# Kernel optimization log

Measured on AMD Instinct MI355X. Metric: run time of the kernel, lower is better.

The kernel has to match this reference:

```python
import jax, jax.numpy as jnp
import numpy as np

B = 512        # batch of parallel sequences
TM1 = 64       # T-1 recurrence steps
BELIEF = 2048  # GRU / deterministic belief size
STATE = 256    # stochastic state size
ACTION = 64
HIDDEN = 2048
EMB = 1024     # embedding_size['fusion']
MIN_STD = 0.1


def setup_inputs() -> dict:
    key = jax.random.key(0)
    ks = jax.random.split(key, 16)
    w = lambda k, shape: jax.random.normal(k, shape, dtype=jnp.float32) * 0.02
    return {
        "prev_state": jax.random.normal(ks[0], (B, STATE), dtype=jnp.float32),
        "actions": jax.random.normal(ks[1], (TM1, B, ACTION), dtype=jnp.float32),
        "prev_belief": jax.random.normal(ks[2], (B, BELIEF), dtype=jnp.float32),
        "obs_emb": jax.random.normal(ks[3], (TM1, B, EMB), dtype=jnp.float32),
        "nonterminals": jnp.ones((TM1, B, 1), dtype=jnp.float32),
        # fc_embed_state_action
        "W_embed": w(ks[4], (STATE + ACTION, BELIEF)),
        "b_embed": jnp.zeros((BELIEF,), jnp.float32),
        # GRUCell (input-to-hidden / hidden-to-hidden, gate order r,z,n as torch)
        "Wi": w(ks[5], (BELIEF, 3 * BELIEF)),
        "bi": jnp.zeros((3 * BELIEF,), jnp.float32),
        "Wh": w(ks[6], (BELIEF, 3 * BELIEF)),
        "bh": jnp.zeros((3 * BELIEF,), jnp.float32),
        # stochastic_state_model (prior): h -> hidden -> 2*state
        "W1": w(ks[7], (BELIEF, HIDDEN)),
        "b1": jnp.zeros((HIDDEN,), jnp.float32),
        "W2": w(ks[8], (HIDDEN, 2 * STATE)),
        "b2": jnp.zeros((2 * STATE,), jnp.float32),
        # obs_encoder (posterior): cat(h, obs_emb) -> hidden -> 2*state
        "W1p": w(ks[9], (BELIEF + EMB, HIDDEN)),
        "b1p": jnp.zeros((HIDDEN,), jnp.float32),
        "W2p": w(ks[10], (HIDDEN, 2 * STATE)),
        "b2p": jnp.zeros((2 * STATE,), jnp.float32),
        # reparameterized-sampling noise (rsample = loc + scale * eps)
        "eps_prior": jax.random.normal(ks[11], (TM1, B, STATE), dtype=jnp.float32),
        "eps_post": jax.random.normal(ks[12], (TM1, B, STATE), dtype=jnp.float32),
    }


def reference(prev_state, actions, prev_belief, obs_emb, nonterminals,
              W_embed, b_embed, Wi, bi, Wh, bh,
              W1, b1, W2, b2, W1p, b1p, W2p, b2p,
              eps_prior, eps_post):
    def step(carry, xs):
        belief, post_state = carry
        a, obs, nt, ep, eq = xs
        s = post_state * nt                                   # [B, S]
        hidden = jax.nn.relu(jnp.concatenate([s, a], axis=1) @ W_embed + b_embed)
        # torch.nn.GRUCell math (gate order r, z, n)
        gi = hidden @ Wi + bi
        gh = belief @ Wh + bh
        i_r, i_z, i_n = jnp.split(gi, 3, axis=1)
        h_r, h_z, h_n = jnp.split(gh, 3, axis=1)
        r = jax.nn.sigmoid(i_r + h_r)
        z = jax.nn.sigmoid(i_z + h_z)
        n = jnp.tanh(i_n + r * h_n)
        new_belief = (1.0 - z) * n + z * belief               # [B, H]
        # prior stochastic state model
        hp = jax.nn.relu(new_belief @ W1 + b1)
        loc_p, raw_p = jnp.split(hp @ W2 + b2, 2, axis=1)
        scale_p = jax.nn.softplus(raw_p) + MIN_STD
        prior_state = loc_p + scale_p * ep                    # rsample
        # posterior from obs embedding
        hq = jax.nn.relu(jnp.concatenate([new_belief, obs], axis=1) @ W1p + b1p)
        loc_q, raw_q = jnp.split(hq @ W2p + b2p, 2, axis=1)
        scale_q = jax.nn.softplus(raw_q) + MIN_STD
        post_new = loc_q + scale_q * eq                       # rsample
        ys = (new_belief, prior_state, loc_p, scale_p, post_new, loc_q, scale_q)
        return (new_belief, post_new), ys

    _, ys = jax.lax.scan(step, (prev_belief, prev_state),
                         (actions, obs_emb, nonterminals, eps_prior, eps_post))
    # (beliefs, prior_states, prior_means, prior_std_devs,
    #  posterior_states, posterior_means, posterior_std_devs), each [T-1, B, ...]
    return ys
```

## Files before the change

### kernel.cpp

```cpp
#include <hip/hip_runtime.h>
#include <hip/hip_bf16.h>
#include <cstdint>

typedef __hip_bfloat16 bf16;
typedef __attribute__((ext_vector_type(8))) short bf16x8v;
typedef __attribute__((ext_vector_type(4))) float f32x4;

#define NB 256
#define NT 512
#define TM1 64

#define OUT_BEL  ((size_t)0)
#define OUT_PST  ((size_t)67108864)
#define OUT_PMU  ((size_t)75497472)
#define OUT_PSD  ((size_t)83886080)
#define OUT_QST  ((size_t)92274688)
#define OUT_QMU  ((size_t)100663296)
#define OUT_QSD  ((size_t)109051904)

__device__ __forceinline__ void gload_lds16(const bf16* g, bf16* l) {
  __builtin_amdgcn_global_load_lds(
      (const __attribute__((address_space(1))) unsigned int*)g,
      (__attribute__((address_space(3))) unsigned int*)l, 16, 0, 0);
}

__device__ __forceinline__ unsigned short bfb(float f) {
  bf16 h = __float2bfloat16(f);
  return *reinterpret_cast<unsigned short*>(&h);
}

__device__ __forceinline__ float sigmoidf_(float x) { return 1.f / (1.f + __expf(-x)); }

__device__ __forceinline__ void gbar(unsigned* bars, unsigned e, int bid) {
  __syncthreads();
  const int g = bid & 7;
  const int tid = threadIdx.x;
  if (tid == 0) {
    __threadfence();
    __hip_atomic_fetch_add(&bars[16 * g], 1u, __ATOMIC_RELAXED, __HIP_MEMORY_SCOPE_AGENT);
  }
  if (bid == 0) {
    if (tid < 8) {
      while (__hip_atomic_load(&bars[16 * tid], __ATOMIC_RELAXED, __HIP_MEMORY_SCOPE_AGENT) < 32u * e)
        __builtin_amdgcn_s_sleep(1);
    }
    __syncthreads();
    if (tid < 8)
      __hip_atomic_store(&bars[128 + 16 * tid], e, __ATOMIC_RELAXED, __HIP_MEMORY_SCOPE_AGENT);
  } else if (tid == 0) {
    while (__hip_atomic_load(&bars[128 + 16 * g], __ATOMIC_RELAXED, __HIP_MEMORY_SCOPE_AGENT) < e)
      __builtin_amdgcn_s_sleep(2);
  }
  if (tid == 0) __threadfence();
  __syncthreads();
}

template<int BM, int BN>
__device__ void gemm_tile(const bf16* __restrict__ A, const bf16* __restrict__ B,
                          const float* __restrict__ bias, void* __restrict__ C,
                          int N, int K, int nm, int mode, int job, int tid,
                          char* pool)
{
  constexpr int LA = BM * 8 / NT;
  constexpr int LB = BN * 8 / NT;
  constexpr int L = LA + LB;
  bf16 (*sA)[BM * 64] = (bf16(*)[BM * 64])pool;
  bf16 (*sB)[BN * 64] = (bf16(*)[BN * 64])(pool + 2 * BM * 64 * 2);

  const int m0 = (job % nm) * BM;
  const int n0 = (job / nm) * BN;
  const int lane = tid & 63;
  const int wid = tid >> 6;
  const int wm = wid >> 1, wn = wid & 1;
  const int lr = lane & 15;
  const int lg = lane >> 4;
  constexpr int WMt = BM / 4, WNt = BN / 2;
  constexpr int MR = WMt / 16, NR = WNt / 16;

  const bf16* Abase = A + (size_t)m0 * K;
  const bf16* Bbase = B + (size_t)n0 * K;

  auto stage = [&](int buf, int k0) {
    #pragma unroll
    for (int i = 0; i < LA; ++i) {
      int c = i * NT + tid;
      int row = c >> 3, kc = c & 7;
      gload_lds16(Abase + (size_t)row * K + k0 + ((kc ^ (row & 7)) << 3), &sA[buf][c * 8]);
    }
    #pragma unroll
    for (int i = 0; i < LB; ++i) {
      int c = i * NT + tid;
      int row = c >> 3, kc = c & 7;
      gload_lds16(Bbase + (size_t)row * K + k0 + ((kc ^ (row & 7)) << 3), &sB[buf][c * 8]);
    }
  };

  f32x4 acc[MR][NR] = {};
  __syncthreads();
  stage(0, 0);
  stage(1, 64);
  const int nk = K >> 6;
  for (int it = 0; it < nk; ++it) {
    const int cur = it & 1;
    if (it + 1 < nk) { asm volatile("s_waitcnt vmcnt(%0)" :: "n"(L) : "memory"); }
    else             { asm volatile("s_waitcnt vmcnt(0)" ::: "memory"); }
    __builtin_amdgcn_sched_barrier(0);
    __builtin_amdgcn_s_barrier();
    __builtin_amdgcn_sched_barrier(0);
    #pragma unroll
    for (int kk = 0; kk < 2; ++kk) {
      const int jg = kk * 4 + lg;
      bf16x8v af[MR], bfv[NR];
      #pragma unroll
      for (int m = 0; m < MR; ++m) {
        int ar = wm * WMt + m * 16 + lr;
        af[m] = *(const bf16x8v*)&sA[cur][ar * 64 + ((jg ^ (ar & 7)) << 3)];
      }
      #pragma unroll
      for (int n = 0; n < NR; ++n) {
        int br = wn * WNt + n * 16 + lr;
        bfv[n] = *(const bf16x8v*)&sB[cur][br * 64 + ((jg ^ (br & 7)) << 3)];
      }
      #pragma unroll
      for (int m = 0; m < MR; ++m)
        #pragma unroll
        for (int n = 0; n < NR; ++n)
          acc[m][n] = __builtin_amdgcn_mfma_f32_16x16x32_bf16(af[m], bfv[n], acc[m][n], 0, 0, 0);
    }
    __builtin_amdgcn_sched_barrier(0);
    __builtin_amdgcn_s_barrier();
    __builtin_amdgcn_sched_barrier(0);
    if (it + 2 < nk) stage(cur, (it + 2) << 6);
  }

  const int r0 = (lane >> 4) * 4;
  #pragma unroll
  for (int m = 0; m < MR; ++m) {
    #pragma unroll
    for (int n = 0; n < NR; ++n) {
      int gc = n0 + wn * WNt + n * 16 + lr;
      float bv = bias[gc];
      #pragma unroll
      for (int r = 0; r < 4; ++r) {
        int gr = m0 + wm * WMt + m * 16 + r0 + r;
        float v = acc[m][n][r] + bv;
        if (mode == 1)
          ((bf16*)C)[(size_t)gr * N + gc] = __float2bfloat16(v > 0.f ? v : 0.f);
        else
          ((float*)C)[(size_t)gr * N + gc] = v;
      }
    }
  }
}

__device__ void fused_gru(const bf16* __restrict__ hidden, const bf16* __restrict__ belsrc,
                          const bf16* __restrict__ WiT, const bf16* __restrict__ WhT,
                          const float* __restrict__ bi, const float* __restrict__ bh,
                          float* __restrict__ belief_f32, float* __restrict__ out_bel,
                          bf16* __restrict__ belslot,
                          int job, int tid, char* pool)
{
  bf16 (*sA)[64 * 64]  = (bf16(*)[64 * 64])pool;
  bf16 (*sB)[192 * 64] = (bf16(*)[192 * 64])(pool + 16384);

  const int m0 = (job & 7) * 64;
  const int j0 = (job >> 3) * 64;
  const int lane = tid & 63;
  const int wid = tid >> 6;
  const int wm = wid >> 2, wn = wid & 3;
  const int lr = lane & 15;
  const int lg = lane >> 4;

  auto stage = [&](int buf, int gt) {
    const bf16* Ab; const bf16* Bb; int k0;
    if (gt < 32) { Ab = hidden; Bb = WiT; k0 = gt << 6; }
    else         { Ab = belsrc; Bb = WhT; k0 = (gt - 32) << 6; }
    {
      int c = tid;
      int row = c >> 3, kc = c & 7;
      gload_lds16(Ab + (size_t)(m0 + row) * 2048 + k0 + ((kc ^ (row & 7)) << 3),
                  &sA[buf][c * 8]);
    }
    #pragma unroll
    for (int i = 0; i < 3; ++i) {
      int c = i * NT + tid;
      int r = c >> 3, kc = c & 7;
      int grow = (r >> 6) * 2048 + j0 + (r & 63);
      gload_lds16(Bb + (size_t)grow * 2048 + k0 + ((kc ^ (r & 7)) << 3),
                  &sB[buf][c * 8]);
    }
  };

  f32x4 ar_[2] = {}, az_[2] = {}, ain[2] = {}, ahn[2] = {};

  auto body = [&](int gt, f32x4 (&ax)[2]) {
    const int cur = gt & 1;
    if (gt < 63) { asm volatile("s_waitcnt vmcnt(4)" ::: "memory"); }
    else         { asm volatile("s_waitcnt vmcnt(0)" ::: "memory"); }
    __builtin_amdgcn_sched_barrier(0);
    __builtin_amdgcn_s_barrier();
    __builtin_amdgcn_sched_barrier(0);
    #pragma unroll
    for (int kk = 0; kk < 2; ++kk) {
      const int jg = kk * 4 + lg;
      bf16x8v af[2], bg[3];
      #pragma unroll
      for (int m = 0; m < 2; ++m) {
        int arow = wm * 32 + m * 16 + lr;
        af[m] = *(const bf16x8v*)&sA[cur][arow * 64 + ((jg ^ (arow & 7)) << 3)];
      }
      #pragma unroll
      for (int g = 0; g < 3; ++g) {
        int br = g * 64 + wn * 16 + lr;
        bg[g] = *(const bf16x8v*)&sB[cur][br * 64 + ((jg ^ (br & 7)) << 3)];
      }
      #pragma unroll
      for (int m = 0; m < 2; ++m) {
        ar_[m] = __builtin_amdgcn_mfma_f32_16x16x32_bf16(af[m], bg[0], ar_[m], 0, 0, 0);
        az_[m] = __builtin_amdgcn_mfma_f32_16x16x32_bf16(af[m], bg[1], az_[m], 0, 0, 0);
        ax[m]  = __builtin_amdgcn_mfma_f32_16x16x32_bf16(af[m], bg[2], ax[m], 0, 0, 0);
      }
    }
    __builtin_amdgcn_sched_barrier(0);
    __builtin_amdgcn_s_barrier();
    __builtin_amdgcn_sched_barrier(0);
    if (gt + 2 < 64) stage(cur, gt + 2);
  };

  __syncthreads();
  stage(0, 0);
  stage(1, 1);
  for (int gt = 0; gt < 32; ++gt) body(gt, ain);
  for (int gt = 32; gt < 64; ++gt) body(gt, ahn);

  const int gc = j0 + wn * 16 + lr;
  const float br_b  = bi[gc] + bh[gc];
  const float bz_b  = bi[2048 + gc] + bh[2048 + gc];
  const float bin_b = bi[4096 + gc];
  const float bhn_b = bh[4096 + gc];
  const int r0 = (lane >> 4) * 4;
  #pragma unroll
  for (int m = 0; m < 2; ++m) {
    #pragma unroll
    for (int r = 0; r < 4; ++r) {
      int grow = m0 + wm * 32 + m * 16 + r0 + r;
      size_t idx = (size_t)grow * 2048 + gc;
      float rr = sigmoidf_(ar_[m][r] + br_b);
      float zz = sigmoidf_(az_[m][r] + bz_b);
      float nn = tanhf(ain[m][r] + bin_b + rr * (ahn[m][r] + bhn_b));
      float bo = belief_f32[idx];
      float nb = (1.f - zz) * nn + zz * bo;
      belief_f32[idx] = nb;
      out_bel[idx] = nb;
      belslot[idx] = __float2bfloat16(nb);
    }
  }
}

__device__ void gemm_w1p(const bf16* __restrict__ Abel, const bf16* __restrict__ Aobs,
                         const bf16* __restrict__ B, const float* __restrict__ bias,
                         bf16* __restrict__ C, int job, int tid, char* pool)
{
  constexpr int K = 3072, NK = 48;
  bf16 (*sA)[64 * 64] = (bf16(*)[64 * 64])pool;
  bf16 (*sB)[64 * 64] = (bf16(*)[64 * 64])(pool + 16384);

  const int m0 = (job & 7) * 64;
  const int n0 = (job >> 3) * 64;
  const int lane = tid & 63;
  const int wid = tid >> 6;
  const int wm = wid >> 1, wn = wid & 1;
  const int lr = lane & 15;
  const int lg = lane >> 4;

  auto stage = [&](int buf, int k0) {
    {
      int c = tid;
      int row = c >> 3, kc = c & 7;
      int sw = (kc ^ (row & 7)) << 3;
      const bf16* src = (k0 < 2048)
          ? Abel + (size_t)(m0 + row) * 2048 + k0 + sw
          : Aobs + (size_t)(m0 + row) * 1024 + (k0 - 2048) + sw;
      gload_lds16(src, &sA[buf][c * 8]);
    }
    {
      int c = tid;
      int row = c >> 3, kc = c & 7;
      gload_lds16(B + (size_t)(n0 + row) * K + k0 + ((kc ^ (row & 7)) << 3), &sB[buf][c * 8]);
    }
  };

  f32x4 acc[2] = {};
  __syncthreads();
  stage(0, 0);
  stage(1, 64);
  for (int it = 0; it < NK; ++it) {
    const int cur = it & 1;
    if (it + 1 < NK) { asm volatile("s_waitcnt vmcnt(2)" ::: "memory"); }
    else             { asm volatile("s_waitcnt vmcnt(0)" ::: "memory"); }
    __builtin_amdgcn_sched_barrier(0);
    __builtin_amdgcn_s_barrier();
    __builtin_amdgcn_sched_barrier(0);
    #pragma unroll
    for (int kk = 0; kk < 2; ++kk) {
      const int jg = kk * 4 + lg;
      int arow = wm * 16 + lr;
      bf16x8v af = *(const bf16x8v*)&sA[cur][arow * 64 + ((jg ^ (arow & 7)) << 3)];
      #pragma unroll
      for (int n = 0; n < 2; ++n) {
        int br = wn * 32 + n * 16 + lr;
        bf16x8v bv = *(const bf16x8v*)&sB[cur][br * 64 + ((jg ^ (br & 7)) << 3)];
        acc[n] = __builtin_amdgcn_mfma_f32_16x16x32_bf16(af, bv, acc[n], 0, 0, 0);
      }
    }
    __builtin_amdgcn_sched_barrier(0);
    __builtin_amdgcn_s_barrier();
    __builtin_amdgcn_sched_barrier(0);
    if (it + 2 < NK) stage(cur, (it + 2) << 6);
  }

  const int r0 = (lane >> 4) * 4;
  #pragma unroll
  for (int n = 0; n < 2; ++n) {
    int gcn = n0 + wn * 32 + n * 16 + lr;
    float bv = bias[gcn];
    #pragma unroll
    for (int r = 0; r < 4; ++r) {
      int gr = m0 + wm * 16 + r0 + r;
      float v = acc[n][r] + bv;
      C[(size_t)gr * 2048 + gcn] = __float2bfloat16(v > 0.f ? v : 0.f);
    }
  }
}

__device__ void w2p_tile(const bf16* __restrict__ hq, const bf16* __restrict__ W2pT,
                         const float* __restrict__ b2p, const float* __restrict__ eps,
                         float* __restrict__ o_mu, float* __restrict__ o_sd,
                         float* __restrict__ o_st,
                         const float* __restrict__ nt_next,
                         const float* __restrict__ act_next,
                         bf16* __restrict__ xcat, int make_xcat,
                         int blk, int tid, char* pool)
{
  constexpr int K = 2048, NK = K / 64;
  const int mb = blk & 7, nl = blk >> 3;
  const int m0 = mb * 64;
  const int j0 = nl * 32;

  bf16 (*sA)[64 * 64] = (bf16(*)[64 * 64])pool;
  bf16 (*sB)[64 * 64] = (bf16(*)[64 * 64])(pool + 16384);
  float* tile = (float*)pool;

  const int lane = tid & 63;
  const int wid = tid >> 6;
  const int wm = wid >> 1, wn = wid & 1;
  const int lr = lane & 15;
  const int lg = lane >> 4;

  const bf16* Abase = hq + (size_t)m0 * K;

  auto stage = [&](int buf, int k0) {
    {
      int c = tid;
      int row = c >> 3, kc = c & 7;
      gload_lds16(Abase + (size_t)row * K + k0 + ((kc ^ (row & 7)) << 3), &sA[buf][c * 8]);
    }
    {
      int c = tid;
      int row = c >> 3, kc = c & 7;
      int grow = (row < 32) ? (j0 + row) : (224 + j0 + row);
      gload_lds16(W2pT + (size_t)grow * K + k0 + ((kc ^ (row & 7)) << 3), &sB[buf][c * 8]);
    }
  };

  f32x4 acc[2] = {};
  __syncthreads();
  stage(0, 0);
  stage(1, 64);
  for (int it = 0; it < NK; ++it) {
    const int cur = it & 1;
    if (it + 1 < NK) { asm volatile("s_waitcnt vmcnt(2)" ::: "memory"); }
    else             { asm volatile("s_waitcnt vmcnt(0)" ::: "memory"); }
    __builtin_amdgcn_sched_barrier(0);
    __builtin_amdgcn_s_barrier();
    __builtin_amdgcn_sched_barrier(0);
    #pragma unroll
    for (int kk = 0; kk < 2; ++kk) {
      const int jg = kk * 4 + lg;
      int ar = wm * 16 + lr;
      bf16x8v af = *(const bf16x8v*)&sA[cur][ar * 64 + ((jg ^ (ar & 7)) << 3)];
      #pragma unroll
      for (int n = 0; n < 2; ++n) {
        int br = wn * 32 + n * 16 + lr;
        bf16x8v bfv = *(const bf16x8v*)&sB[cur][br * 64 + ((jg ^ (br & 7)) << 3)];
        acc[n] = __builtin_amdgcn_mfma_f32_16x16x32_bf16(af, bfv, acc[n], 0, 0, 0);
      }
    }
    __builtin_amdgcn_sched_barrier(0);
    __builtin_amdgcn_s_barrier();
    __builtin_amdgcn_sched_barrier(0);
    if (it + 2 < NK) stage(cur, (it + 2) << 6);
  }

  const int r0 = (lane >> 4) * 4;
  #pragma unroll
  for (int n = 0; n < 2; ++n) {
    int tc = wn * 32 + n * 16 + lr;
    #pragma unroll
    for (int r = 0; r < 4; ++r)
      tile[(wm * 16 + r0 + r) * 64 + tc] = acc[n][r];
  }
  __syncthreads();

  for (int e = tid; e < 64 * 32; e += NT) {
    int rr = e >> 5, cc = e & 31;
    int b = m0 + rr;
    int j = j0 + cc;
    float loc = tile[rr * 64 + cc] + b2p[j];
    float raw = tile[rr * 64 + 32 + cc] + b2p[256 + j];
    float sp = (raw > 20.f) ? raw : log1pf(__expf(raw));
    float scale = sp + 0.1f;
    float st = loc + scale * eps[(size_t)b * 256 + j];
    o_mu[(size_t)b * 256 + j] = loc;
    o_sd[(size_t)b * 256 + j] = scale;
    o_st[(size_t)b * 256 + j] = st;
    if (make_xcat)
      xcat[(size_t)b * 320 + j] = __float2bfloat16(st * nt_next[b]);
  }
  if (make_xcat && nl == 0) {
    for (int e = tid; e < 64 * 64; e += NT) {
      int rr = e >> 6, cc = e & 63;
      int b = m0 + rr;
      xcat[(size_t)b * 320 + 256 + cc] = __float2bfloat16(act_next[(size_t)b * 64 + cc]);
    }
  }
}

__device__ void transpose_phase(const float* __restrict__ src, bf16* __restrict__ dst,
                                int K, int N, int bid, int tid, float* t )
{
  const int ntile = (K / 32) * (N / 32);
  const int tx = tid & 31, ty = tid >> 5;
  for (int it = bid; it < ntile; it += NB) {
    int kt = it % (K / 32), nt = it / (K / 32);
    int k0 = kt * 32, n0 = nt * 32;
    __syncthreads();
    #pragma unroll
    for (int i = 0; i < 32; i += 16)
      t[(ty + i) * 33 + tx] = src[(size_t)(k0 + ty + i) * N + n0 + tx];
    __syncthreads();
    #pragma unroll
    for (int i = 0; i < 32; i += 16)
      dst[(size_t)(n0 + ty + i) * K + k0 + tx] = __float2bfloat16(t[tx * 33 + ty + i]);
  }
}

struct Args {
  const float *prev_state, *actions, *prev_belief, *obs_emb, *nonterm;
  const float *W_embed, *b_embed, *Wi, *bi, *Wh, *bh;
  const float *W1, *b1, *W2, *b2, *W1p, *b1p, *W2p, *b2p;
  const float *eps_p, *eps_q;
  bf16 *WembT, *WiT, *WhT, *W1T, *W2T, *W1pT, *W2pT;
  float* belief_f32; bf16 *bel_init, *xcat, *hidden, *obsB;
  bf16 *hq, *belA, *hp; float* yp;
  float* out;
  unsigned* cnt;
};

__global__ __launch_bounds__(NT, 2) void mega(Args a)
{
  extern __shared__ char pool[];
  const int bid = blockIdx.x;
  const int tid = threadIdx.x;
  const int sj = ((bid & 7) << 5) | (bid >> 3);
  unsigned ep = 0;

  transpose_phase(a.W_embed, a.WembT, 320, 2048, bid, tid, (float*)pool);
  transpose_phase(a.Wi,  a.WiT,  2048, 6144, bid, tid, (float*)pool);
  transpose_phase(a.Wh,  a.WhT,  2048, 6144, bid, tid, (float*)pool);
  transpose_phase(a.W1,  a.W1T,  2048, 2048, bid, tid, (float*)pool);
  transpose_phase(a.W2,  a.W2T,  2048, 512,  bid, tid, (float*)pool);
  transpose_phase(a.W1p, a.W1pT, 3072, 2048, bid, tid, (float*)pool);
  transpose_phase(a.W2p, a.W2pT, 2048, 512,  bid, tid, (float*)pool);
  for (int i = bid * NT + tid; i < 512 * 2048; i += NB * NT) {
    float v = a.prev_belief[i];
    a.belief_f32[i] = v;
    a.bel_init[i] = __float2bfloat16(v);
  }
  for (int i = bid * NT + tid; i < 512 * 320; i += NB * NT) {
    int b = i / 320, c = i - b * 320;
    float v = (c < 256) ? a.prev_state[b * 256 + c] * a.nonterm[b]
                        : a.actions[b * 64 + (c - 256)];
    a.xcat[i] = __float2bfloat16(v);
  }
  for (int i = bid * NT + tid; i < TM1 * 512 * 1024 / 4; i += NB * NT) {
    float4 v = *(const float4*)&a.obs_emb[(size_t)i * 4];
    ushort4 u; u.x = bfb(v.x); u.y = bfb(v.y); u.z = bfb(v.z); u.w = bfb(v.w);
    *(ushort4*)&a.obsB[(size_t)i * 4] = u;
  }
  gbar(a.cnt, ++ep, bid);

  gemm_tile<64, 64>(a.xcat, a.WembT, a.b_embed, a.hidden, 2048, 320, 8, 1, sj, tid, pool);
  gbar(a.cnt, ++ep, bid);

  for (int t = 0; t < TM1; ++t) {
    const bf16* belsrc = (t == 0) ? a.bel_init : a.belA + (size_t)(t - 1) * 512 * 2048;
    fused_gru(a.hidden, belsrc, a.WiT, a.WhT, a.bi, a.bh,
              a.belief_f32,
              a.out + OUT_BEL + (size_t)t * 512 * 2048,
              a.belA + (size_t)t * 512 * 2048,
              sj, tid, pool);
    gbar(a.cnt, ++ep, bid);

    gemm_w1p(a.belA + (size_t)t * 512 * 2048,
             a.obsB + (size_t)t * 512 * 1024,
             a.W1pT, a.b1p, a.hq, sj, tid, pool);
    gbar(a.cnt, ++ep, bid);

    {
      int tn = (t < TM1 - 1) ? t + 1 : t;
      if (bid < 64)
        w2p_tile(a.hq, a.W2pT, a.b2p,
                 a.eps_q + (size_t)t * 512 * 256,
                 a.out + OUT_QMU + (size_t)t * 512 * 256,
                 a.out + OUT_QSD + (size_t)t * 512 * 256,
                 a.out + OUT_QST + (size_t)t * 512 * 256,
                 a.nonterm + (size_t)tn * 512,
                 a.actions + (size_t)tn * 512 * 64,
                 a.xcat, (t < TM1 - 1) ? 1 : 0, bid, tid, pool);
    }
    gbar(a.cnt, ++ep, bid);

    if (t < TM1 - 1) {
      gemm_tile<64, 64>(a.xcat, a.WembT, a.b_embed, a.hidden, 2048, 320, 8, 1, sj, tid, pool);
      gbar(a.cnt, ++ep, bid);
    }
  }

  for (int ch = 0; ch < 8; ++ch) {
    const bf16* Ach = a.belA + (size_t)ch * 4096 * 2048;
    for (int r = 0; r < 2; ++r) {
      int j = r * NB + sj;
      if (j < 512)
        gemm_tile<128, 128>(Ach, a.W1T, a.b1, a.hp, 2048, 2048, 32, 1, j, tid, pool);
    }
    gbar(a.cnt, ++ep, bid);

    if (sj < 128)
      gemm_tile<128, 128>(a.hp, a.W2T, a.b2, a.yp, 512, 2048, 32, 0, sj, tid, pool);
    gbar(a.cnt, ++ep, bid);

    for (int i = bid * NT + tid; i < 4096 * 256; i += NB * NT) {
      int r = i >> 8, j = i & 255;
      float loc = a.yp[(size_t)r * 512 + j];
      float raw = a.yp[(size_t)r * 512 + 256 + j];
      float sp = (raw > 20.f) ? raw : log1pf(__expf(raw));
      float scale = sp + 0.1f;
      size_t o = (size_t)ch * 4096 * 256 + i;
      a.out[OUT_PMU + o] = loc;
      a.out[OUT_PSD + o] = scale;
      a.out[OUT_PST + o] = loc + scale * a.eps_p[o];
    }
    gbar(a.cnt, ++ep, bid);
  }
}

extern "C" void kernel_launch(void* const* d_in, const int* in_sizes, int n_in,
                              void* d_out, int out_size, void* d_ws, size_t ws_size,
                              hipStream_t stream)
{
  (void)in_sizes; (void)n_in; (void)out_size; (void)ws_size;
  Args a;
  a.prev_state = (const float*)d_in[0];
  a.actions    = (const float*)d_in[1];
  a.prev_belief= (const float*)d_in[2];
  a.obs_emb    = (const float*)d_in[3];
  a.nonterm    = (const float*)d_in[4];
  a.W_embed    = (const float*)d_in[5];
  a.b_embed    = (const float*)d_in[6];
  a.Wi         = (const float*)d_in[7];
  a.bi         = (const float*)d_in[8];
  a.Wh         = (const float*)d_in[9];
  a.bh         = (const float*)d_in[10];
  a.W1         = (const float*)d_in[11];
  a.b1         = (const float*)d_in[12];
  a.W2         = (const float*)d_in[13];
  a.b2         = (const float*)d_in[14];
  a.W1p        = (const float*)d_in[15];
  a.b1p        = (const float*)d_in[16];
  a.W2p        = (const float*)d_in[17];
  a.b2p        = (const float*)d_in[18];
  a.eps_p      = (const float*)d_in[19];
  a.eps_q      = (const float*)d_in[20];
  a.out        = (float*)d_out;

  char* ws = (char*)d_ws;
  size_t off = 0;
  auto alloc = [&](size_t bytes) -> char* {
    char* p = ws + off;
    off = (off + bytes + 255) & ~(size_t)255;
    return p;
  };
  a.cnt        = (unsigned*)alloc(4096);
  a.WembT      = (bf16*)alloc((size_t)2048 * 320 * 2);
  a.WiT        = (bf16*)alloc((size_t)6144 * 2048 * 2);
  a.WhT        = (bf16*)alloc((size_t)6144 * 2048 * 2);
  a.W1T        = (bf16*)alloc((size_t)2048 * 2048 * 2);
  a.W2T        = (bf16*)alloc((size_t)512 * 2048 * 2);
  a.W1pT       = (bf16*)alloc((size_t)2048 * 3072 * 2);
  a.W2pT       = (bf16*)alloc((size_t)512 * 2048 * 2);
  a.belief_f32 = (float*)alloc((size_t)512 * 2048 * 4);
  a.bel_init   = (bf16*)alloc((size_t)512 * 2048 * 2);
  a.xcat       = (bf16*)alloc((size_t)512 * 320 * 2);
  a.hidden     = (bf16*)alloc((size_t)512 * 2048 * 2);
  a.obsB       = (bf16*)alloc((size_t)TM1 * 512 * 1024 * 2);
  a.hq         = (bf16*)alloc((size_t)512 * 2048 * 2);
  a.belA       = (bf16*)alloc((size_t)TM1 * 512 * 2048 * 2);
  a.hp         = (bf16*)alloc((size_t)4096 * 2048 * 2);
  a.yp         = (float*)alloc((size_t)4096 * 512 * 4);

  hipMemsetAsync(a.cnt, 0, 4096, stream);
  mega<<<NB, NT, 65536, stream>>>(a);
}
```

Measured before the change: 8.673 ms.

## Enlarge GEMM tiles, add triple-buffered W1p pipeline, and use fewer active blocks

The GRU, W1p and embedding GEMMs move from 64x64-class tiles to 128x128 tiles, and the prior-model GEMMs move to 256x256 tiles. Dynamic LDS is raised to 128 KB to hold the larger tiles, and the W1p GEMM gets a three-deep load pipeline. The goal is to raise MFMA work per loaded byte and cut redundant weight reads across row tiles. The trade-off is that each phase now has only 32–128 jobs instead of 256, so many CUs sit idle while per-block latency grows.

Result: slower. 18.15 ms (+109.3%).

```diff
diff --git a/kernel.cpp b/kernel.cpp
--- a/kernel.cpp
+++ b/kernel.cpp
@@ -31,6 +31,10 @@
 
 __device__ __forceinline__ float sigmoidf_(float x) { return 1.f / (1.f + __expf(-x)); }
 
+__device__ __forceinline__ int jid(int bid, int nj) {
+  return (bid < nj) ? ((bid & 7) * (nj >> 3) + (bid >> 3)) : -1;
+}
+
 __device__ __forceinline__ void gbar(unsigned* bars, unsigned e, int bid) {
   __syncthreads();
   const int g = bid & 7;
@@ -55,7 +59,7 @@
   __syncthreads();
 }
 
-template<int BM, int BN>
+template<int BM, int BN, int DEPTH>
 __device__ void gemm_tile(const bf16* __restrict__ A, const bf16* __restrict__ B,
                           const float* __restrict__ bias, void* __restrict__ C,
                           int N, int K, int nm, int mode, int job, int tid,
@@ -64,8 +68,10 @@
   constexpr int LA = BM * 8 / NT;
   constexpr int LB = BN * 8 / NT;
   constexpr int L = LA + LB;
-  bf16 (*sA)[BM * 64] = (bf16(*)[BM * 64])pool;
-  bf16 (*sB)[BN * 64] = (bf16(*)[BN * 64])(pool + 2 * BM * 64 * 2);
+  constexpr int WMt = BM / 4, WNt = BN / 2;
+  constexpr int MR = WMt / 16, NR = WNt / 16;
+  bf16* sAb = (bf16*)pool;
+  bf16* sBb = (bf16*)(pool + (size_t)DEPTH * BM * 64 * 2);
 
   const int m0 = (job % nm) * BM;
   const int n0 = (job / nm) * BN;
@@ -74,39 +80,48 @@
   const int wm = wid >> 1, wn = wid & 1;
   const int lr = lane & 15;
   const int lg = lane >> 4;
-  constexpr int WMt = BM / 4, WNt = BN / 2;
-  constexpr int MR = WMt / 16, NR = WNt / 16;
 
   const bf16* Abase = A + (size_t)m0 * K;
   const bf16* Bbase = B + (size_t)n0 * K;
 
   auto stage = [&](int buf, int k0) {
+    bf16* dA = sAb + buf * (BM * 64);
+    bf16* dB = sBb + buf * (BN * 64);
     #pragma unroll
     for (int i = 0; i < LA; ++i) {
       int c = i * NT + tid;
       int row = c >> 3, kc = c & 7;
-      gload_lds16(Abase + (size_t)row * K + k0 + ((kc ^ (row & 7)) << 3), &sA[buf][c * 8]);
+      gload_lds16(Abase + (size_t)row * K + k0 + ((kc ^ (row & 7)) << 3), &dA[c * 8]);
     }
     #pragma unroll
     for (int i = 0; i < LB; ++i) {
       int c = i * NT + tid;
       int row = c >> 3, kc = c & 7;
-      gload_lds16(Bbase + (size_t)row * K + k0 + ((kc ^ (row & 7)) << 3), &sB[buf][c * 8]);
+      gload_lds16(Bbase + (size_t)row * K + k0 + ((kc ^ (row & 7)) << 3), &dB[c * 8]);
     }
   };
 
   f32x4 acc[MR][NR] = {};
   __syncthreads();
-  stage(0, 0);
-  stage(1, 64);
   const int nk = K >> 6;
+  #pragma unroll
+  for (int d = 0; d < DEPTH; ++d)
+    if (d < nk) stage(d, d << 6);
+  int cur = 0;
   for (int it = 0; it < nk; ++it) {
-    const int cur = it & 1;
-    if (it + 1 < nk) { asm volatile("s_waitcnt vmcnt(%0)" :: "n"(L) : "memory"); }
-    else             { asm volatile("s_waitcnt vmcnt(0)" ::: "memory"); }
-    __builtin_amdgcn_sched_barrier(0);
-    __builtin_amdgcn_s_barrier();
-    __builtin_amdgcn_sched_barrier(0);
+    if (DEPTH == 3) {
+      if (it + 2 < nk)      { asm volatile("s_waitcnt vmcnt(%0)" :: "n"(2 * L) : "memory"); }
+      else if (it + 1 < nk) { asm volatile("s_waitcnt vmcnt(%0)" :: "n"(L) : "memory"); }
+      else                  { asm volatile("s_waitcnt vmcnt(0)" ::: "memory"); }
+    } else {
+      if (it + 1 < nk)      { asm volatile("s_waitcnt vmcnt(%0)" :: "n"(L) : "memory"); }
+      else                  { asm volatile("s_waitcnt vmcnt(0)" ::: "memory"); }
+    }
+    __builtin_amdgcn_sched_barrier(0);
+    __builtin_amdgcn_s_barrier();
+    __builtin_amdgcn_sched_barrier(0);
+    const bf16* cA = sAb + cur * (BM * 64);
+    const bf16* cB = sBb + cur * (BN * 64);
     #pragma unroll
     for (int kk = 0; kk < 2; ++kk) {
       const int jg = kk * 4 + lg;
@@ -114,12 +129,12 @@
       #pragma unroll
       for (int m = 0; m < MR; ++m) {
         int ar = wm * WMt + m * 16 + lr;
-        af[m] = *(const bf16x8v*)&sA[cur][ar * 64 + ((jg ^ (ar & 7)) << 3)];
+        af[m] = *(const bf16x8v*)&cA[ar * 64 + ((jg ^ (ar & 7)) << 3)];
       }
       #pragma unroll
       for (int n = 0; n < NR; ++n) {
         int br = wn * WNt + n * 16 + lr;
-        bfv[n] = *(const bf16x8v*)&sB[cur][br * 64 + ((jg ^ (br & 7)) << 3)];
+        bfv[n] = *(const bf16x8v*)&cB[br * 64 + ((jg ^ (br & 7)) << 3)];
       }
       #pragma unroll
       for (int m = 0; m < MR; ++m)
@@ -130,7 +145,8 @@
     __builtin_amdgcn_sched_barrier(0);
     __builtin_amdgcn_s_barrier();
     __builtin_amdgcn_sched_barrier(0);
-    if (it + 2 < nk) stage(cur, (it + 2) << 6);
+    if (it + DEPTH < nk) stage(cur, (it + DEPTH) << 6);
+    cur = (cur + 1 == DEPTH) ? 0 : cur + 1;
   }
 
   const int r0 = (lane >> 4) * 4;
@@ -160,14 +176,14 @@
                           bf16* __restrict__ belslot,
                           int job, int tid, char* pool)
 {
-  bf16 (*sA)[64 * 64]  = (bf16(*)[64 * 64])pool;
-  bf16 (*sB)[192 * 64] = (bf16(*)[192 * 64])(pool + 16384);
-
-  const int m0 = (job & 7) * 64;
-  const int j0 = (job >> 3) * 64;
+  bf16 (*sA)[128 * 64] = (bf16(*)[128 * 64])pool;
+  bf16 (*sB)[384 * 64] = (bf16(*)[384 * 64])(pool + 32768);
+
+  const int m0 = (job & 3) * 128;
+  const int j0 = (job >> 2) * 128;
   const int lane = tid & 63;
   const int wid = tid >> 6;
-  const int wm = wid >> 2, wn = wid & 3;
+  const int wm = wid >> 1, wn = wid & 1;
   const int lr = lane & 15;
   const int lg = lane >> 4;
 
@@ -175,27 +191,28 @@
     const bf16* Ab; const bf16* Bb; int k0;
     if (gt < 32) { Ab = hidden; Bb = WiT; k0 = gt << 6; }
     else         { Ab = belsrc; Bb = WhT; k0 = (gt - 32) << 6; }
-    {
-      int c = tid;
+    #pragma unroll
+    for (int i = 0; i < 2; ++i) {
+      int c = i * NT + tid;
       int row = c >> 3, kc = c & 7;
       gload_lds16(Ab + (size_t)(m0 + row) * 2048 + k0 + ((kc ^ (row & 7)) << 3),
                   &sA[buf][c * 8]);
     }
     #pragma unroll
-    for (int i = 0; i < 3; ++i) {
+    for (int i = 0; i < 6; ++i) {
       int c = i * NT + tid;
       int r = c >> 3, kc = c & 7;
-      int grow = (r >> 6) * 2048 + j0 + (r & 63);
+      int grow = (r >> 7) * 2048 + j0 + (r & 127);
       gload_lds16(Bb + (size_t)grow * 2048 + k0 + ((kc ^ (r & 7)) << 3),
                   &sB[buf][c * 8]);
     }
   };
 
-  f32x4 ar_[2] = {}, az_[2] = {}, ain[2] = {}, ahn[2] = {};
-
-  auto body = [&](int gt, f32x4 (&ax)[2]) {
+  f32x4 ar_[2][4] = {}, az_[2][4] = {}, ain[2][4] = {}, ahn[2][4] = {};
+
+  auto body = [&](int gt, f32x4 (&ax)[2][4]) {
     const int cur = gt & 1;
-    if (gt < 63) { asm volatile("s_waitcnt vmcnt(4)" ::: "memory"); }
+    if (gt < 63) { asm volatile("s_waitcnt vmcnt(8)" ::: "memory"); }
     else         { asm volatile("s_waitcnt vmcnt(0)" ::: "memory"); }
     __builtin_amdgcn_sched_barrier(0);
     __builtin_amdgcn_s_barrier();
@@ -203,23 +220,27 @@
     #pragma unroll
     for (int kk = 0; kk < 2; ++kk) {
       const int jg = kk * 4 + lg;
-      bf16x8v af[2], bg[3];
+      bf16x8v af[2], bg[3][4];
       #pragma unroll
       for (int m = 0; m < 2; ++m) {
         int arow = wm * 32 + m * 16 + lr;
         af[m] = *(const bf16x8v*)&sA[cur][arow * 64 + ((jg ^ (arow & 7)) << 3)];
       }
       #pragma unroll
-      for (int g = 0; g < 3; ++g) {
-        int br = g * 64 + wn * 16 + lr;
-        bg[g] = *(const bf16x8v*)&sB[cur][br * 64 + ((jg ^ (br & 7)) << 3)];
-      }
-      #pragma unroll
-      for (int m = 0; m < 2; ++m) {
-        ar_[m] = __builtin_amdgcn_mfma_f32_16x16x32_bf16(af[m], bg[0], ar_[m], 0, 0, 0);
-        az_[m] = __builtin_amdgcn_mfma_f32_16x16x32_bf16(af[m], bg[1], az_[m], 0, 0, 0);
-        ax[m]  = __builtin_amdgcn_mfma_f32_16x16x32_bf16(af[m], bg[2], ax[m], 0, 0, 0);
-      }
+      for (int g = 0; g < 3; ++g)
+        #pragma unroll
+        for (int n = 0; n < 4; ++n) {
+          int br = g * 128 + wn * 64 + n * 16 + lr;
+          bg[g][n] = *(const bf16x8v*)&sB[cur][br * 64 + ((jg ^ (br & 7)) << 3)];
+        }
+      #pragma unroll
+      for (int m = 0; m < 2; ++m)
+        #pragma unroll
+        for (int n = 0; n < 4; ++n) {
+          ar_[m][n] = __builtin_amdgcn_mfma_f32_16x16x32_bf16(af[m], bg[0][n], ar_[m][n], 0, 0, 0);
+          az_[m][n] = __builtin_amdgcn_mfma_f32_16x16x32_bf16(af[m], bg[1][n], az_[m][n], 0, 0, 0);
+          ax[m][n]  = __builtin_amdgcn_mfma_f32_16x16x32_bf16(af[m], bg[2][n], ax[m][n], 0, 0, 0);
+        }
     }
     __builtin_amdgcn_sched_barrier(0);
     __builtin_amdgcn_s_barrier();
@@ -233,26 +254,29 @@
   for (int gt = 0; gt < 32; ++gt) body(gt, ain);
   for (int gt = 32; gt < 64; ++gt) body(gt, ahn);
 
-  const int gc = j0 + wn * 16 + lr;
-  const float br_b  = bi[gc] + bh[gc];
-  const float bz_b  = bi[2048 + gc] + bh[2048 + gc];
-  const float bin_b = bi[4096 + gc];
-  const float bhn_b = bh[4096 + gc];
   const int r0 = (lane >> 4) * 4;
   #pragma unroll
-  for (int m = 0; m < 2; ++m) {
-    #pragma unroll
-    for (int r = 0; r < 4; ++r) {
-      int grow = m0 + wm * 32 + m * 16 + r0 + r;
-      size_t idx = (size_t)grow * 2048 + gc;
-      float rr = sigmoidf_(ar_[m][r] + br_b);
-      float zz = sigmoidf_(az_[m][r] + bz_b);
-      float nn = tanhf(ain[m][r] + bin_b + rr * (ahn[m][r] + bhn_b));
-      float bo = belief_f32[idx];
-      float nb = (1.f - zz) * nn + zz * bo;
-      belief_f32[idx] = nb;
-      out_bel[idx] = nb;
-      belslot[idx] = __float2bfloat16(nb);
+  for (int n = 0; n < 4; ++n) {
+    const int gc = j0 + wn * 64 + n * 16 + lr;
+    const float br_b  = bi[gc] + bh[gc];
+    const float bz_b  = bi[2048 + gc] + bh[2048 + gc];
+    const float bin_b = bi[4096 + gc];
+    const float bhn_b = bh[4096 + gc];
+    #pragma unroll
+    for (int m = 0; m < 2; ++m) {
+      #pragma unroll
+      for (int r = 0; r < 4; ++r) {
+        int grow = m0 + wm * 32 + m * 16 + r0 + r;
+        size_t idx = (size_t)grow * 2048 + gc;
+        float rr = sigmoidf_(ar_[m][n][r] + br_b);
+        float zz = sigmoidf_(az_[m][n][r] + bz_b);
+        float nn = tanhf(ain[m][n][r] + bin_b + rr * (ahn[m][n][r] + bhn_b));
+        float bo = belief_f32[idx];
+        float nb = (1.f - zz) * nn + zz * bo;
+        belief_f32[idx] = nb;
+        out_bel[idx] = nb;
+        belslot[idx] = __float2bfloat16(nb);
+      }
     }
   }
 }
@@ -262,11 +286,11 @@
                          bf16* __restrict__ C, int job, int tid, char* pool)
 {
   constexpr int K = 3072, NK = 48;
-  bf16 (*sA)[64 * 64] = (bf16(*)[64 * 64])pool;
-  bf16 (*sB)[64 * 64] = (bf16(*)[64 * 64])(pool + 16384);
-
-  const int m0 = (job & 7) * 64;
-  const int n0 = (job >> 3) * 64;
+  bf16* sAb = (bf16*)pool;
+  bf16* sBb = (bf16*)(pool + 49152);
+
+  const int m0 = (job & 3) * 128;
+  const int n0 = (job >> 2) * 128;
   const int lane = tid & 63;
   const int wid = tid >> 6;
   const int wm = wid >> 1, wn = wid & 1;
@@ -274,62 +298,79 @@
   const int lg = lane >> 4;
 
   auto stage = [&](int buf, int k0) {
-    {
-      int c = tid;
+    bf16* dA = sAb + buf * (128 * 64);
+    bf16* dB = sBb + buf * (128 * 64);
+    #pragma unroll
+    for (int i = 0; i < 2; ++i) {
+      int c = i * NT + tid;
       int row = c >> 3, kc = c & 7;
       int sw = (kc ^ (row & 7)) << 3;
       const bf16* src = (k0 < 2048)
           ? Abel + (size_t)(m0 + row) * 2048 + k0 + sw
           : Aobs + (size_t)(m0 + row) * 1024 + (k0 - 2048) + sw;
-      gload_lds16(src, &sA[buf][c * 8]);
-    }
-    {
-      int c = tid;
+      gload_lds16(src, &dA[c * 8]);
+    }
+    #pragma unroll
+    for (int i = 0; i < 2; ++i) {
+      int c = i * NT + tid;
       int row = c >> 3, kc = c & 7;
-      gload_lds16(B + (size_t)(n0 + row) * K + k0 + ((kc ^ (row & 7)) << 3), &sB[buf][c * 8]);
+      gload_lds16(B + (size_t)(n0 + row) * K + k0 + ((kc ^ (row & 7)) << 3), &dB[c * 8]);
     }
   };
 
-  f32x4 acc[2] = {};
+  f32x4 acc[2][4] = {};
   __syncthreads();
-  stage(0, 0);
-  stage(1, 64);
+  stage(0, 0); stage(1, 64); stage(2, 128);
+  int cur = 0;
   for (int it = 0; it < NK; ++it) {
-    const int cur = it & 1;
-    if (it + 1 < NK) { asm volatile("s_waitcnt vmcnt(2)" ::: "memory"); }
-    else             { asm volatile("s_waitcnt vmcnt(0)" ::: "memory"); }
-    __builtin_amdgcn_sched_barrier(0);
-    __builtin_amdgcn_s_barrier();
-    __builtin_amdgcn_sched_barrier(0);
+    if (it + 2 < NK)      { asm volatile("s_waitcnt vmcnt(8)" ::: "memory"); }
+    else if (it + 1 < NK) { asm volatile("s_waitcnt vmcnt(4)" ::: "memory"); }
+    else                  { asm volatile("s_waitcnt vmcnt(0)" ::: "memory"); }
+    __builtin_amdgcn_sched_barrier(0);
+    __builtin_amdgcn_s_barrier();
+    __builtin_amdgcn_sched_barrier(0);
+    const bf16* cA = sAb + cur * (128 * 64);
+    const bf16* cB = sBb + cur * (128 * 64);
     #pragma unroll
     for (int kk = 0; kk < 2; ++kk) {
       const int jg = kk * 4 + lg;
-      int arow = wm * 16 + lr;
-      bf16x8v af = *(const bf16x8v*)&sA[cur][arow * 64 + ((jg ^ (arow & 7)) << 3)];
-      #pragma unroll
-      for (int n = 0; n < 2; ++n) {
-        int br = wn * 32 + n * 16 + lr;
-        bf16x8v bv = *(const bf16x8v*)&sB[cur][br * 64 + ((jg ^ (br & 7)) << 3)];
-        acc[n] = __builtin_amdgcn_mfma_f32_16x16x32_bf16(af, bv, acc[n], 0, 0, 0);
-      }
-    }
-    __builtin_amdgcn_sched_barrier(0);
-    __builtin_amdgcn_s_barrier();
-    __builtin_amdgcn_sched_barrier(0);
-    if (it + 2 < NK) stage(cur, (it + 2) << 6);
+      bf16x8v af[2], bfv[4];
+      #pragma unroll
+      for (int m = 0; m < 2; ++m) {
+        int ar = wm * 32 + m * 16 + lr;
+        af[m] = *(const bf16x8v*)&cA[ar * 64 + ((jg ^ (ar & 7)) << 3)];
+      }
+      #pragma unroll
+      for (int n = 0; n < 4; ++n) {
+        int br = wn * 64 + n * 16 + lr;
+        bfv[n] = *(const bf16x8v*)&cB[br * 64 + ((jg ^ (br & 7)) << 3)];
+      }
+      #pragma unroll
+      for (int m = 0; m < 2; ++m)
+        #pragma unroll
+        for (int n = 0; n < 4; ++n)
+          acc[m][n] = __builtin_amdgcn_mfma_f32_16x16x32_bf16(af[m], bfv[n], acc[m][n], 0, 0, 0);
+    }
+    __builtin_amdgcn_sched_barrier(0);
+    __builtin_amdgcn_s_barrier();
+    __builtin_amdgcn_sched_barrier(0);
+    if (it + 3 < NK) stage(cur, (it + 3) << 6);
+    cur = (cur + 1 == 3) ? 0 : cur + 1;
   }
 
   const int r0 = (lane >> 4) * 4;
   #pragma unroll
-  for (int n = 0; n < 2; ++n) {
-    int gcn = n0 + wn * 32 + n * 16 + lr;
+  for (int n = 0; n < 4; ++n) {
+    int gcn = n0 + wn * 64 + n * 16 + lr;
     float bv = bias[gcn];
     #pragma unroll
-    for (int r = 0; r < 4; ++r) {
-      int gr = m0 + wm * 16 + r0 + r;
-      float v = acc[n][r] + bv;
-      C[(size_t)gr * 2048 + gcn] = __float2bfloat16(v > 0.f ? v : 0.f);
-    }
+    for (int m = 0; m < 2; ++m)
+      #pragma unroll
+      for (int r = 0; r < 4; ++r) {
+        int gr = m0 + wm * 32 + m * 16 + r0 + r;
+        float v = acc[m][n][r] + bv;
+        C[(size_t)gr * 2048 + gcn] = __float2bfloat16(v > 0.f ? v : 0.f);
+      }
   }
 }
 
@@ -472,7 +513,6 @@
   extern __shared__ char pool[];
   const int bid = blockIdx.x;
   const int tid = threadIdx.x;
-  const int sj = ((bid & 7) << 5) | (bid >> 3);
   unsigned ep = 0;
 
   transpose_phase(a.W_embed, a.WembT, 320, 2048, bid, tid, (float*)pool);
@@ -500,21 +540,33 @@
   }
   gbar(a.cnt, ++ep, bid);
 
-  gemm_tile<64, 64>(a.xcat, a.WembT, a.b_embed, a.hidden, 2048, 320, 8, 1, sj, tid, pool);
+  {
+    int j = jid(bid, 64);
+    if (j >= 0)
+      gemm_tile<128, 128, 2>(a.xcat, a.WembT, a.b_embed, a.hidden, 2048, 320, 4, 1, j, tid, pool);
+  }
   gbar(a.cnt, ++ep, bid);
 
   for (int t = 0; t < TM1; ++t) {
     const bf16* belsrc = (t == 0) ? a.bel_init : a.belA + (size_t)(t - 1) * 512 * 2048;
-    fused_gru(a.hidden, belsrc, a.WiT, a.WhT, a.bi, a.bh,
-              a.belief_f32,
-              a.out + OUT_BEL + (size_t)t * 512 * 2048,
-              a.belA + (size_t)t * 512 * 2048,
-              sj, tid, pool);
+    {
+      int j = jid(bid, 64);
+      if (j >= 0)
+        fused_gru(a.hidden, belsrc, a.WiT, a.WhT, a.bi, a.bh,
+                  a.belief_f32,
+                  a.out + OUT_BEL + (size_t)t * 512 * 2048,
+                  a.belA + (size_t)t * 512 * 2048,
+                  j, tid, pool);
+    }
     gbar(a.cnt, ++ep, bid);
 
-    gemm_w1p(a.belA + (size_t)t * 512 * 2048,
-             a.obsB + (size_t)t * 512 * 1024,
-             a.W1pT, a.b1p, a.hq, sj, tid, pool);
+    {
+      int j = jid(bid, 64);
+      if (j >= 0)
+        gemm_w1p(a.belA + (size_t)t * 512 * 2048,
+                 a.obsB + (size_t)t * 512 * 1024,
+                 a.W1pT, a.b1p, a.hq, j, tid, pool);
+    }
     gbar(a.cnt, ++ep, bid);
 
     {
@@ -532,22 +584,27 @@
     gbar(a.cnt, ++ep, bid);
 
     if (t < TM1 - 1) {
-      gemm_tile<64, 64>(a.xcat, a.WembT, a.b_embed, a.hidden, 2048, 320, 8, 1, sj, tid, pool);
+      int j = jid(bid, 64);
+      if (j >= 0)
+        gemm_tile<128, 128, 2>(a.xcat, a.WembT, a.b_embed, a.hidden, 2048, 320, 4, 1, j, tid, pool);
       gbar(a.cnt, ++ep, bid);
     }
   }
 
   for (int ch = 0; ch < 8; ++ch) {
     const bf16* Ach = a.belA + (size_t)ch * 4096 * 2048;
-    for (int r = 0; r < 2; ++r) {
-      int j = r * NB + sj;
-      if (j < 512)
-        gemm_tile<128, 128>(Ach, a.W1T, a.b1, a.hp, 2048, 2048, 32, 1, j, tid, pool);
+    {
+      int j = jid(bid, 128);
+      if (j >= 0)
+        gemm_tile<256, 256, 2>(Ach, a.W1T, a.b1, a.hp, 2048, 2048, 16, 1, j, tid, pool);
     }
     gbar(a.cnt, ++ep, bid);
 
-    if (sj < 128)
-      gemm_tile<128, 128>(a.hp, a.W2T, a.b2, a.yp, 512, 2048, 32, 0, sj, tid, pool);
+    {
+      int j = jid(bid, 32);
+      if (j >= 0)
+        gemm_tile<256, 256, 2>(a.hp, a.W2T, a.b2, a.yp, 512, 2048, 16, 0, j, tid, pool);
+    }
     gbar(a.cnt, ++ep, bid);
 
     for (int i = bid * NT + tid; i < 4096 * 256; i += NB * NT) {
@@ -619,6 +676,8 @@
   a.hp         = (bf16*)alloc((size_t)4096 * 2048 * 2);
   a.yp         = (float*)alloc((size_t)4096 * 512 * 4);
 
+  hipFuncSetAttribute((const void*)mega,
+                      hipFuncAttributeMaxDynamicSharedMemorySize, 131072);
   hipMemsetAsync(a.cnt, 0, 4096, stream);
-  mega<<<NB, NT, 65536, stream>>>(a);
-}
+  mega<<<NB, NT, 131072, stream>>>(a);
+}
```
